# Kernel optimization log

Hardware: AMD Instinct MI355X
Metric: run time of the kernel (lower is better)

The kernel has to match this reference:

```python
import jax, jax.numpy as jnp
import numpy as np

DIM_HEAD = 64
HEADS = 16
EMBED = DIM_HEAD * HEADS
FF = 2 * EMBED
SCALE_BASE = 512.0
LN_EPS = 1e-5
L2_EPS = 1e-12


def setup_inputs() -> dict:
    key = jax.random.key(0)
    ks = jax.random.split(key, 12)
    B, S = 4, 2048
    inp = {
        "Q": jax.random.normal(ks[0], (B, S, EMBED), jnp.float32),
        "K": jax.random.normal(ks[1], (B, S, EMBED), jnp.float32),
        "V": jax.random.normal(ks[2], (B, S, EMBED), jnp.float32),
        "Wqkv": jax.random.normal(ks[3], (EMBED, 3 * EMBED), jnp.float32) * (EMBED ** -0.5),
        "bqkv": jnp.zeros((3 * EMBED,), jnp.float32),
        "q_scale": jnp.ones((DIM_HEAD,), jnp.float32),
        "k_scale": jnp.ones((DIM_HEAD,), jnp.float32),
        "ln_g": jnp.ones((EMBED,), jnp.float32),
        "ln_b": jnp.zeros((EMBED,), jnp.float32),
        "W1": jax.random.normal(ks[4], (EMBED, FF), jnp.float32) * (EMBED ** -0.5),
        "b1": jnp.zeros((FF,), jnp.float32),
        "W2": jax.random.normal(ks[5], (FF, EMBED), jnp.float32) * (FF ** -0.5),
        "b2": jnp.zeros((EMBED,), jnp.float32),
    }
    return inp


def rotate_half(x):
    x1, x2 = jnp.split(x, 2, axis=-1)
    return jnp.concatenate((-x2, x1), axis=-1)


def rotary_tables(seq_len, dim):
    t = jnp.arange(seq_len, dtype=jnp.float32)
    inv_freq = 1.0 / (10000.0 ** (jnp.arange(0, dim, 2, dtype=jnp.float32) / dim))
    freqs = t[:, None] * inv_freq[None, :]            # [S, dim/2]
    freqs = jnp.concatenate((freqs, freqs), axis=-1)  # [S, dim]
    base = (jnp.arange(0, dim, 2, dtype=jnp.float32) + 0.4 * dim) / (1.4 * dim)
    power = (t - seq_len // 2) / SCALE_BASE
    scale = base[None, :] ** power[:, None]           # [S, dim/2]
    scale = jnp.concatenate((scale, scale), axis=-1)  # [S, dim]
    return freqs, scale


def reference(Q, K, V, Wqkv, bqkv, q_scale, k_scale, ln_g, ln_b, W1, b1, W2, b2):
    B, S, D = Q.shape
    dh = q_scale.shape[0]
    H = D // dh

    qkv = Q @ Wqkv + bqkv                              # [B,S,3D]
    qkv = qkv.reshape(B, S, H, 3 * dh).transpose(0, 2, 1, 3)  # [B,H,S,3dh]
    q, k, v = jnp.split(qkv, 3, axis=-1)

    # l2 normalize along head dim (F.normalize semantics)
    q = q / jnp.maximum(jnp.linalg.norm(q, axis=-1, keepdims=True), L2_EPS)
    k = k / jnp.maximum(jnp.linalg.norm(k, axis=-1, keepdims=True), L2_EPS)
    q = q * q_scale
    k = k * k_scale

    freqs, scale = rotary_tables(S, dh)
    cos, sin = jnp.cos(freqs), jnp.sin(freqs)
    q = q * cos * scale + rotate_half(q) * sin * scale
    inv_scale = 1.0 / scale
    k = k * cos * inv_scale + rotate_half(k) * sin * inv_scale

    # scaled dot product attention (non-causal, default scale 1/sqrt(dh))
    logits = jnp.einsum('bhqd,bhkd->bhqk', q, k) / jnp.sqrt(jnp.float32(dh))
    attn = jax.nn.softmax(logits, axis=-1)
    out = jnp.einsum('bhqk,bhkd->bhqd', attn, v)       # [B,H,S,dh]
    out = out.transpose(0, 2, 1, 3).reshape(B, S, D)

    mu = jnp.mean(out, axis=-1, keepdims=True)
    var = jnp.var(out, axis=-1, keepdims=True)
    x = (out - mu) * jax.lax.rsqrt(var + LN_EPS) * ln_g + ln_b

    ff = jax.nn.silu(x @ W1 + b1) @ W2 + b2
    return x + ff
```

## Files before the change

kernel.cpp:

```cpp
#include <hip/hip_runtime.h>
#include <hip/hip_bf16.h>
#include <math.h>


typedef __bf16 bf16_t;
typedef __bf16 bf16x8 __attribute__((ext_vector_type(8)));
typedef _Float16 f16_t;
typedef _Float16 f16x8 __attribute__((ext_vector_type(8)));
typedef float  f32x4  __attribute__((ext_vector_type(4)));

#define B_  4
#define S_  2048
#define H_  16
#define DH_ 64
#define D_  1024
#define FF_ 2048
#define M_  (B_ * S_)

__device__ __forceinline__ float ldx(const void* p, int i, int f) {
    return f ? ((const float*)p)[i] : (float)((const bf16_t*)p)[i];
}
__device__ __forceinline__ float b2f(unsigned short u) {
    return (float)__builtin_bit_cast(bf16_t, u);
}
__device__ __forceinline__ void gll16(const void* g, const void* lds) {
    __builtin_amdgcn_global_load_lds(
        (const __attribute__((address_space(1))) unsigned int*)g,
        (__attribute__((address_space(3))) unsigned int*)lds, 16, 0, 0);
}

__global__ void detect_k(const unsigned short* q, int n, int* flag) {
    const int tid = threadIdx.x;
    float cnt = 0.f;
    for (int i = tid; i < n; i += 256) {
        const int e = (q[i] >> 7) & 0xFF;
        if (e >= 134) cnt += 1.f;
    }
    __shared__ float red[256];
    red[tid] = cnt;
    __syncthreads();
    for (int s = 128; s > 0; s >>= 1) {
        if (tid < s) red[tid] += red[tid + s];
        __syncthreads();
    }
    if (tid == 0) { flag[0] = (red[0] > 0.5f) ? 1 : 0; flag[1] = 1; }
}

__global__ void rope_tables_k(float* __restrict__ ct, float* __restrict__ st,
                              float* __restrict__ sct) {
    const int s = blockIdx.x, i = threadIdx.x;
    const float inv_freq = powf(10000.f, -(float)i / 32.f);
    const float f = (float)s * inv_freq;
    ct[s * 32 + i] = cosf(f);
    st[s * 32 + i] = sinf(f);
    const float base = (2.f * (float)i + 25.6f) / 89.6f;
    const float pw = ((float)s - 1024.f) / 512.f;
    sct[s * 32 + i] = powf(base, pw);
}

__global__ __launch_bounds__(256)
void cvt16_k(const void* __restrict__ in, const int* __restrict__ flag,
             f16_t* __restrict__ o, int n8) {
    const int id = blockIdx.x * 256 + threadIdx.x;
    if (id >= n8) return;
    f16x8 v;
    if (flag[0]) {
        const float4 a = ((const float4*)in)[id * 2];
        const float4 b = ((const float4*)in)[id * 2 + 1];
        v[0] = (f16_t)a.x; v[1] = (f16_t)a.y; v[2] = (f16_t)a.z; v[3] = (f16_t)a.w;
        v[4] = (f16_t)b.x; v[5] = (f16_t)b.y; v[6] = (f16_t)b.z; v[7] = (f16_t)b.w;
    } else {
        const ushort4 a = ((const ushort4*)in)[id * 2];
        const ushort4 b = ((const ushort4*)in)[id * 2 + 1];
        v[0] = (f16_t)b2f(a.x); v[1] = (f16_t)b2f(a.y); v[2] = (f16_t)b2f(a.z); v[3] = (f16_t)b2f(a.w);
        v[4] = (f16_t)b2f(b.x); v[5] = (f16_t)b2f(b.y); v[6] = (f16_t)b2f(b.z); v[7] = (f16_t)b2f(b.w);
    }
    ((f16x8*)o)[id] = v;
}

__global__ __launch_bounds__(256)
void prep_wt16_k(const void* __restrict__ W, const int* __restrict__ flag,
                 f16_t* __restrict__ T16, int K, int N) {
    __shared__ float T[32][33];
    const int tid = threadIdx.x;
    const int n0 = blockIdx.x * 32, k0 = blockIdx.y * 32;
    const int f = flag[0];
#pragma unroll
    for (int i = 0; i < 4; ++i) {
        const int p = i * 256 + tid;
        const int r = p >> 5, c = p & 31;
        T[c][r] = ldx(W, (k0 + r) * N + n0 + c, f);
    }
    __syncthreads();
#pragma unroll
    for (int i = 0; i < 4; ++i) {
        const int p = i * 256 + tid;
        const int r = p >> 5, c = p & 31;
        T16[(size_t)(n0 + r) * K + k0 + c] = (f16_t)T[r][c];
    }
}

template <int ACT, int OUT16, bool RES>
__global__ __launch_bounds__(256)
void gemm16_k(const f16_t* __restrict__ A16, const f16_t* __restrict__ B16,
              const void* __restrict__ bias, const int* __restrict__ fbias,
              const float* __restrict__ resid, float* __restrict__ C,
              f16_t* __restrict__ C16, int M, int N, int K) {
    __shared__ __align__(16) f16_t As[128 * 32];
    __shared__ __align__(16) f16_t Bs[128 * 32];
    const int tid = threadIdx.x;
    const int lane = tid & 63, w = tid >> 6;
    const int l15 = lane & 15, l4 = lane >> 4;
    const int wm = w >> 1, wn = w & 1;
    const int bm = blockIdx.y * 128, bn = blockIdx.x * 128;
    const int sr = lane >> 2, sc = lane & 3;
    const int ck = sc ^ ((sr >> 1) & 3);
    const int rsel = (l15 >> 1) & 3;
    (void)M;

    f32x4 acc[4][4];
#pragma unroll
    for (int i = 0; i < 4; ++i)
#pragma unroll
        for (int j = 0; j < 4; ++j) acc[i][j] = (f32x4){0.f, 0.f, 0.f, 0.f};

    for (int k0 = 0; k0 < K; k0 += 32) {
        __syncthreads();
#pragma unroll
        for (int i = 0; i < 2; ++i) {
            const int t = w * 2 + i;
            const int r = t * 16 + sr;
            gll16(A16 + (size_t)(bm + r) * K + k0 + ck * 8, As + t * 512);
            gll16(B16 + (size_t)(bn + r) * K + k0 + ck * 8, Bs + t * 512);
        }
        __syncthreads();
        f16x8 af[4], bfr[4];
#pragma unroll
        for (int i = 0; i < 4; ++i) {
            const int r = wm * 64 + i * 16 + l15;
            af[i] = *(const f16x8*)&As[r * 32 + ((l4 ^ rsel) << 3)];
        }
#pragma unroll
        for (int j = 0; j < 4; ++j) {
            const int r = wn * 64 + j * 16 + l15;
            bfr[j] = *(const f16x8*)&Bs[r * 32 + ((l4 ^ rsel) << 3)];
        }
#pragma unroll
        for (int i = 0; i < 4; ++i)
#pragma unroll
            for (int j = 0; j < 4; ++j)
                acc[i][j] = __builtin_amdgcn_mfma_f32_16x16x32_f16(af[i], bfr[j], acc[i][j], 0, 0, 0);
    }

    const int fc = fbias[0];
#pragma unroll
    for (int j = 0; j < 4; ++j) {
        const int col = bn + wn * 64 + j * 16 + l15;
        const float bv = ldx(bias, col, fc);
#pragma unroll
        for (int i = 0; i < 4; ++i) {
            const int row0 = bm + wm * 64 + i * 16 + l4 * 4;
#pragma unroll
            for (int r = 0; r < 4; ++r) {
                float t = acc[i][j][r] + bv;
                if constexpr (ACT == 1) t = t / (1.f + expf(-t));
                if constexpr (RES) t += resid[(size_t)(row0 + r) * N + col];
                if constexpr (OUT16) C16[(size_t)(row0 + r) * N + col] = (f16_t)t;
                else                 C[(size_t)(row0 + r) * N + col] = t;
            }
        }
    }
}

__global__ __launch_bounds__(256)
void qkv_post_k(float* __restrict__ qkv,
                const void* __restrict__ qsc, const void* __restrict__ ksc,
                const int* __restrict__ flag,
                const float* __restrict__ ct, const float* __restrict__ st,
                const float* __restrict__ sct, bf16_t* __restrict__ Kb) {
    const int id = blockIdx.x * 256 + threadIdx.x;
    if (id >= M_ * H_) return;
    const int f = flag[0];
    const int bs = id >> 4, h = id & 15;
    const int s = bs & (S_ - 1), b = bs >> 11;
    float* row = qkv + (size_t)bs * (3 * D_) + h * 192;

    float q[DH_];
    float n2 = 0.f;
#pragma unroll
    for (int d = 0; d < DH_; ++d) { q[d] = row[d]; n2 += q[d] * q[d]; }
    float inv = 1.f / fmaxf(sqrtf(n2), 1e-12f);
#pragma unroll
    for (int d = 0; d < DH_; ++d) q[d] *= inv * ldx(qsc, d, f);
#pragma unroll
    for (int d = 0; d < 32; ++d) {
        const float c = ct[s * 32 + d], sn = st[s * 32 + d], sc = sct[s * 32 + d];
        const float a = q[d], bb = q[d + 32];
        q[d]      = (a * c - bb * sn) * sc;
        q[d + 32] = (bb * c + a * sn) * sc;
    }
#pragma unroll
    for (int d = 0; d < DH_; ++d) row[d] = q[d];
    n2 = 0.f;
#pragma unroll
    for (int d = 0; d < DH_; ++d) { q[d] = row[64 + d]; n2 += q[d] * q[d]; }
    inv = 1.f / fmaxf(sqrtf(n2), 1e-12f);
#pragma unroll
    for (int d = 0; d < DH_; ++d) q[d] *= inv * ldx(ksc, d, f);
#pragma unroll
    for (int d = 0; d < 32; ++d) {
        const float c = ct[s * 32 + d], sn = st[s * 32 + d], isc = 1.f / sct[s * 32 + d];
        const float a = q[d], bb = q[d + 32];
        q[d]      = (a * c - bb * sn) * isc;
        q[d + 32] = (bb * c + a * sn) * isc;
    }
    bf16_t* kr = Kb + ((size_t)(b * H_ + h) * S_ + s) * DH_;
#pragma unroll
    for (int d8 = 0; d8 < 8; ++d8) {
        bf16x8 v;
#pragma unroll
        for (int j = 0; j < 8; ++j) v[j] = (bf16_t)q[d8 * 8 + j];
        *(bf16x8*)(kr + d8 * 8) = v;
    }
}

__global__ __launch_bounds__(256)
void vtrans_k(const float* __restrict__ qkv, bf16_t* __restrict__ Vt) {
    __shared__ float T[32][65];
    const int tid = threadIdx.x;
    const int s0 = blockIdx.x * 32;
    const int h  = blockIdx.y;
    const int b  = blockIdx.z;
    {
        const int r = tid >> 3, d0 = (tid & 7) * 8;
        const float* vrow = qkv + (size_t)(b * S_ + s0 + r) * (3 * D_) + h * 192 + 128;
        const float4 a = *(const float4*)(vrow + d0);
        const float4 c = *(const float4*)(vrow + d0 + 4);
        T[r][d0 + 0] = a.x; T[r][d0 + 1] = a.y; T[r][d0 + 2] = a.z; T[r][d0 + 3] = a.w;
        T[r][d0 + 4] = c.x; T[r][d0 + 5] = c.y; T[r][d0 + 6] = c.z; T[r][d0 + 7] = c.w;
    }
    __syncthreads();
    {
        const int d = tid >> 2, sl0 = (tid & 3) * 8;
        bf16x8 o;
#pragma unroll
        for (int j = 0; j < 8; ++j) o[j] = (bf16_t)T[sl0 + j][d];
        *(bf16x8*)(Vt + ((size_t)(b * H_ + h) * DH_ + d) * S_ + s0 + sl0) = o;
    }
}

__global__ __launch_bounds__(256)
void attn_mfma_k(const float* __restrict__ qkv, const bf16_t* __restrict__ Kb,
                 const bf16_t* __restrict__ Vt, float* __restrict__ att) {
    constexpr int RS = 72;
    __shared__ __align__(16) bf16_t Ks[64 * RS];
    __shared__ __align__(16) bf16_t Vs[64 * RS];
    __shared__ __align__(16) bf16_t Ps[4][16 * RS];
    const int tid = threadIdx.x;
    const int lane = tid & 63, w = tid >> 6;
    const int l15 = lane & 15, l4 = lane >> 4;
    const int bid = blockIdx.x;
    const int bh = (bid & 7) * 8 + (bid >> 8);
    const int qt = (bid >> 3) & 31;
    const int b = bh >> 4, h = bh & 15;
    const int q0 = qt * 64 + w * 16;

    bf16x8 qf[2];
    {
        const float* qrow = qkv + (size_t)(b * S_ + q0 + l15) * (3 * D_) + h * 192;
#pragma unroll
        for (int t = 0; t < 2; ++t) {
            const float4 v0 = *(const float4*)(qrow + t * 32 + l4 * 8);
            const float4 v1 = *(const float4*)(qrow + t * 32 + l4 * 8 + 4);
            bf16x8 q8;
            q8[0] = (bf16_t)(v0.x * 0.125f); q8[1] = (bf16_t)(v0.y * 0.125f);
            q8[2] = (bf16_t)(v0.z * 0.125f); q8[3] = (bf16_t)(v0.w * 0.125f);
            q8[4] = (bf16_t)(v1.x * 0.125f); q8[5] = (bf16_t)(v1.y * 0.125f);
            q8[6] = (bf16_t)(v1.z * 0.125f); q8[7] = (bf16_t)(v1.w * 0.125f);
            qf[t] = q8;
        }
    }
    f32x4 of[4];
#pragma unroll
    for (int i = 0; i < 4; ++i) of[i] = (f32x4){0.f, 0.f, 0.f, 0.f};
    float psum[4] = {0.f, 0.f, 0.f, 0.f};

    const bf16_t* Kg = Kb + (size_t)bh * S_ * DH_;
    const bf16_t* Vg = Vt + (size_t)bh * DH_ * S_;
    const int sr = tid >> 2, sc = (tid & 3) * 16;

    for (int j0 = 0; j0 < S_; j0 += 64) {
        __syncthreads();
        *(bf16x8*)&Ks[sr * RS + sc]     = *(const bf16x8*)(Kg + (size_t)(j0 + sr) * DH_ + sc);
        *(bf16x8*)&Ks[sr * RS + sc + 8] = *(const bf16x8*)(Kg + (size_t)(j0 + sr) * DH_ + sc + 8);
        *(bf16x8*)&Vs[sr * RS + sc]     = *(const bf16x8*)(Vg + (size_t)sr * S_ + j0 + sc);
        *(bf16x8*)&Vs[sr * RS + sc + 8] = *(const bf16x8*)(Vg + (size_t)sr * S_ + j0 + sc + 8);
        __syncthreads();

        f32x4 sf[4];
#pragma unroll
        for (int i = 0; i < 4; ++i) sf[i] = (f32x4){0.f, 0.f, 0.f, 0.f};
#pragma unroll
        for (int t = 0; t < 2; ++t)
#pragma unroll
            for (int fj = 0; fj < 4; ++fj) {
                const bf16x8 kf = *(const bf16x8*)&Ks[(fj * 16 + l15) * RS + t * 32 + l4 * 8];
                sf[fj] = __builtin_amdgcn_mfma_f32_16x16x32_bf16(qf[t], kf, sf[fj], 0, 0, 0);
            }
#pragma unroll
        for (int fj = 0; fj < 4; ++fj)
#pragma unroll
            for (int r = 0; r < 4; ++r) {
                const float p = __expf(sf[fj][r]);
                const bf16_t pb = (bf16_t)p;
                psum[r] += (float)pb;
                Ps[w][(l4 * 4 + r) * RS + fj * 16 + l15] = pb;
            }
#pragma unroll
        for (int t = 0; t < 2; ++t) {
            const bf16x8 pf = *(const bf16x8*)&Ps[w][l15 * RS + t * 32 + l4 * 8];
#pragma unroll
            for (int fd = 0; fd < 4; ++fd) {
                const bf16x8 vf = *(const bf16x8*)&Vs[(fd * 16 + l15) * RS + t * 32 + l4 * 8];
                of[fd] = __builtin_amdgcn_mfma_f32_16x16x32_bf16(pf, vf, of[fd], 0, 0, 0);
            }
        }
    }
#pragma unroll
    for (int r = 0; r < 4; ++r)
#pragma unroll
        for (int msk = 1; msk < 16; msk <<= 1) psum[r] += __shfl_xor(psum[r], msk);
#pragma unroll
    for (int r = 0; r < 4; ++r) {
        const float inv = 1.f / psum[r];
        float* orow = att + (size_t)(b * S_ + q0 + l4 * 4 + r) * D_ + h * DH_;
#pragma unroll
        for (int fd = 0; fd < 4; ++fd) orow[fd * 16 + l15] = of[fd][r] * inv;
    }
}

__global__ __launch_bounds__(256)
void layernorm_k(const float* __restrict__ in, const void* __restrict__ g,
                 const void* __restrict__ be, const int* __restrict__ flag,
                 float* __restrict__ xo, f16_t* __restrict__ x16) {
    const int row = blockIdx.x, tid = threadIdx.x;
    const int lane = tid & 63, wave = tid >> 6;
    const int f = flag[0];
    const float* r = in + (size_t)row * D_;
    float v[4], s = 0.f, ss = 0.f;
#pragma unroll
    for (int i = 0; i < 4; ++i) {
        v[i] = r[tid + i * 256];
        s += v[i]; ss += v[i] * v[i];
    }
#pragma unroll
    for (int msk = 1; msk < 64; msk <<= 1) { s += __shfl_xor(s, msk); ss += __shfl_xor(ss, msk); }
    __shared__ float rs[4], rss[4];
    if (lane == 0) { rs[wave] = s; rss[wave] = ss; }
    __syncthreads();
    s = rs[0] + rs[1] + rs[2] + rs[3];
    ss = rss[0] + rss[1] + rss[2] + rss[3];
    const float mu = s * (1.f / (float)D_);
    const float var = fmaxf(ss * (1.f / (float)D_) - mu * mu, 0.f);
    const float inv = rsqrtf(var + 1e-5f);
    float* xr = xo + (size_t)row * D_;
    f16_t* hr = x16 + (size_t)row * D_;
#pragma unroll
    for (int i = 0; i < 4; ++i) {
        const int c = tid + i * 256;
        const float t = (v[i] - mu) * inv * ldx(g, c, f) + ldx(be, c, f);
        xr[c] = t;
        hr[c] = (f16_t)t;
    }
}

__global__ void host_marker_k(int code, float* __restrict__ out) {
    if (code != 0) out[0] = 1e10f * (float)(1 + code);
}

extern "C" void kernel_launch(void* const* d_in, const int* in_sizes, int n_in,
                              void* d_out, int out_size, void* d_ws, size_t ws_size,
                              hipStream_t stream) {
    (void)out_size;
    const void* Q    = d_in[0];
    const void* Wqkv = d_in[3];
    const void* bqkv = d_in[4];
    const void* qsc  = d_in[5];
    const void* ksc  = d_in[6];
    const void* ln_g = d_in[7];
    const void* ln_b = d_in[8];
    const void* W1   = d_in[9];
    const void* b1   = d_in[10];
    const void* W2   = d_in[11];
    const void* b2   = d_in[12];

    constexpr size_t OFF_QKV  = 0;
    constexpr size_t OFF_X    = 0;
    constexpr size_t OFF_X16  = 33554432;
    constexpr size_t OFF_H16  = 50331648;
    constexpr size_t OFF_WQ16 = 100663296;
    constexpr size_t OFF_W116 = 106954752;
    constexpr size_t OFF_W216 = 111149056;
    constexpr size_t OFF_Q16  = 115343360;
    constexpr size_t OFF_KB   = 115343360;
    constexpr size_t OFF_VT   = 132120576;
    constexpr size_t OFF_RC   = 148897792;
    constexpr size_t OFF_RS   = OFF_RC + 262144;
    constexpr size_t OFF_RSC  = OFF_RS + 262144;
    constexpr size_t OFF_FLAG = OFF_RSC + 262144;
    constexpr size_t WS_NEED  = OFF_FLAG + 64;

    float* out = (float*)d_out;
    char* ws = (char*)d_ws;
    float*  qkv   = (float*)(ws + OFF_QKV);
    float*  xbuf  = (float*)(ws + OFF_X);
    f16_t*  x16   = (f16_t*)(ws + OFF_X16);
    f16_t*  h16   = (f16_t*)(ws + OFF_H16);
    f16_t*  wq16  = (f16_t*)(ws + OFF_WQ16);
    f16_t*  w116  = (f16_t*)(ws + OFF_W116);
    f16_t*  w216  = (f16_t*)(ws + OFF_W216);
    f16_t*  q16   = (f16_t*)(ws + OFF_Q16);
    bf16_t* kb    = (bf16_t*)(ws + OFF_KB);
    bf16_t* vtb   = (bf16_t*)(ws + OFF_VT);
    float*  rc    = (float*)(ws + OFF_RC);
    float*  rsn   = (float*)(ws + OFF_RS);
    float*  rsc   = (float*)(ws + OFF_RSC);
    int*    flag  = (int*)(ws + OFF_FLAG);

    int err_stage = 0;
    (void)hipGetLastError();
    #define LCHK(stage) do { if (hipGetLastError() != hipSuccess && err_stage == 0) err_stage = (stage); } while (0)

    if (n_in != 13) err_stage = 90;
    else if (in_sizes[0] != 8388608 || in_sizes[3] != 3145728 || in_sizes[4] != 3072 ||
             in_sizes[5] != 64 || in_sizes[7] != 1024 || in_sizes[9] != 2097152 ||
             in_sizes[10] != 2048 || in_sizes[11] != 2097152 || in_sizes[12] != 1024)
        err_stage = 91;
    else if (ws_size < WS_NEED) err_stage = 92;
    if (err_stage != 0) {
        host_marker_k<<<1, 1, 0, stream>>>(err_stage, out);
        return;
    }

    detect_k<<<1, 256, 0, stream>>>((const unsigned short*)Q, 65536, flag);        LCHK(1);
    rope_tables_k<<<S_, 32, 0, stream>>>(rc, rsn, rsc);                            LCHK(2);
    cvt16_k<<<(M_ * D_ / 8) / 256, 256, 0, stream>>>(Q, flag, q16, M_ * D_ / 8);   LCHK(3);
    prep_wt16_k<<<dim3(3 * D_ / 32, D_ / 32), 256, 0, stream>>>(
        Wqkv, flag, wq16, D_, 3 * D_);                                             LCHK(4);
    prep_wt16_k<<<dim3(FF_ / 32, D_ / 32), 256, 0, stream>>>(
        W1, flag, w116, D_, FF_);                                                  LCHK(5);
    prep_wt16_k<<<dim3(D_ / 32, FF_ / 32), 256, 0, stream>>>(
        W2, flag, w216, FF_, D_);                                                  LCHK(6);
    gemm16_k<0, 0, false><<<dim3(3 * D_ / 128, M_ / 128), 256, 0, stream>>>(
        q16, wq16, bqkv, flag, nullptr, qkv, nullptr, M_, 3 * D_, D_);             LCHK(7);
    qkv_post_k<<<(M_ * H_) / 256, 256, 0, stream>>>(
        qkv, qsc, ksc, flag, rc, rsn, rsc, kb);                                    LCHK(8);
    vtrans_k<<<dim3(S_ / 32, H_, B_), 256, 0, stream>>>(qkv, vtb);                 LCHK(9);
    attn_mfma_k<<<B_ * H_ * (S_ / 64), 256, 0, stream>>>(qkv, kb, vtb, out);       LCHK(10);
    layernorm_k<<<M_, 256, 0, stream>>>(out, ln_g, ln_b, flag, xbuf, x16);         LCHK(11);
    gemm16_k<1, 1, false><<<dim3(FF_ / 128, M_ / 128), 256, 0, stream>>>(
        x16, w116, b1, flag, nullptr, nullptr, h16, M_, FF_, D_);                  LCHK(12);
    gemm16_k<0, 0, true><<<dim3(D_ / 128, M_ / 128), 256, 0, stream>>>(
        h16, w216, b2, flag, xbuf, out, nullptr, M_, D_, FF_);                     LCHK(13);
    host_marker_k<<<1, 1, 0, stream>>>(err_stage, out);
    #undef LCHK
}
```

Before: 658.8 us.

## Store QKV in fp16, pre-scale Q to bf16, double-buffer attention K/V with async loads

The QKV GEMM now writes fp16 instead of fp32, and the post-processing kernel writes Q as pre-scaled bf16 in a head-major layout. The attention kernel therefore reads compact Q directly and stages K/V with direct global-to-LDS loads into a double buffer. The LDS tiles use XOR swizzles instead of padding, and the MFMA sections get wave priority hints. LayerNorm no longer writes an fp32 copy, and the final GEMM takes its residual from the fp16 normalized tensor. Together these cut memory traffic and overlap loads with compute, at the cost of some precision in the QKV intermediate and the residual.

```diff
diff --git a/kernel.cpp b/kernel.cpp
--- a/kernel.cpp
+++ b/kernel.cpp
@@ -100,12 +100,12 @@
     }
 }
 
-template <int ACT, int OUT16, bool RES>
+template <int ACT, int OUT16, int RES>
 __global__ __launch_bounds__(256)
 void gemm16_k(const f16_t* __restrict__ A16, const f16_t* __restrict__ B16,
               const void* __restrict__ bias, const int* __restrict__ fbias,
-              const float* __restrict__ resid, float* __restrict__ C,
-              f16_t* __restrict__ C16, int M, int N, int K) {
+              const float* __restrict__ residf, const f16_t* __restrict__ resid16,
+              float* __restrict__ C, f16_t* __restrict__ C16, int M, int N, int K) {
     __shared__ __align__(16) f16_t As[128 * 32];
     __shared__ __align__(16) f16_t Bs[128 * 32];
     const int tid = threadIdx.x;
@@ -164,7 +164,8 @@
             for (int r = 0; r < 4; ++r) {
                 float t = acc[i][j][r] + bv;
                 if constexpr (ACT == 1) t = t / (1.f + expf(-t));
-                if constexpr (RES) t += resid[(size_t)(row0 + r) * N + col];
+                if constexpr (RES == 1) t += residf[(size_t)(row0 + r) * N + col];
+                if constexpr (RES == 2) t += (float)resid16[(size_t)(row0 + r) * N + col];
                 if constexpr (OUT16) C16[(size_t)(row0 + r) * N + col] = (f16_t)t;
                 else                 C[(size_t)(row0 + r) * N + col] = t;
             }
@@ -173,22 +174,27 @@
 }
 
 __global__ __launch_bounds__(256)
-void qkv_post_k(float* __restrict__ qkv,
+void qkv_post_k(const f16_t* __restrict__ qkv16,
                 const void* __restrict__ qsc, const void* __restrict__ ksc,
                 const int* __restrict__ flag,
                 const float* __restrict__ ct, const float* __restrict__ st,
-                const float* __restrict__ sct, bf16_t* __restrict__ Kb) {
+                const float* __restrict__ sct,
+                bf16_t* __restrict__ Qb, bf16_t* __restrict__ Kb) {
     const int id = blockIdx.x * 256 + threadIdx.x;
     if (id >= M_ * H_) return;
     const int f = flag[0];
     const int bs = id >> 4, h = id & 15;
     const int s = bs & (S_ - 1), b = bs >> 11;
-    float* row = qkv + (size_t)bs * (3 * D_) + h * 192;
+    const f16_t* row = qkv16 + (size_t)bs * (3 * D_) + h * 192;
 
     float q[DH_];
     float n2 = 0.f;
 #pragma unroll
-    for (int d = 0; d < DH_; ++d) { q[d] = row[d]; n2 += q[d] * q[d]; }
+    for (int d8 = 0; d8 < 8; ++d8) {
+        const f16x8 v = *(const f16x8*)(row + d8 * 8);
+#pragma unroll
+        for (int j = 0; j < 8; ++j) { q[d8 * 8 + j] = (float)v[j]; n2 += q[d8*8+j]*q[d8*8+j]; }
+    }
     float inv = 1.f / fmaxf(sqrtf(n2), 1e-12f);
 #pragma unroll
     for (int d = 0; d < DH_; ++d) q[d] *= inv * ldx(qsc, d, f);
@@ -199,11 +205,21 @@
         q[d]      = (a * c - bb * sn) * sc;
         q[d + 32] = (bb * c + a * sn) * sc;
     }
-#pragma unroll
-    for (int d = 0; d < DH_; ++d) row[d] = q[d];
+    bf16_t* qr = Qb + ((size_t)(b * H_ + h) * S_ + s) * DH_;
+#pragma unroll
+    for (int d8 = 0; d8 < 8; ++d8) {
+        bf16x8 v;
+#pragma unroll
+        for (int j = 0; j < 8; ++j) v[j] = (bf16_t)(q[d8 * 8 + j] * 0.125f);
+        *(bf16x8*)(qr + d8 * 8) = v;
+    }
     n2 = 0.f;
 #pragma unroll
-    for (int d = 0; d < DH_; ++d) { q[d] = row[64 + d]; n2 += q[d] * q[d]; }
+    for (int d8 = 0; d8 < 8; ++d8) {
+        const f16x8 v = *(const f16x8*)(row + 64 + d8 * 8);
+#pragma unroll
+        for (int j = 0; j < 8; ++j) { q[d8 * 8 + j] = (float)v[j]; n2 += q[d8*8+j]*q[d8*8+j]; }
+    }
     inv = 1.f / fmaxf(sqrtf(n2), 1e-12f);
 #pragma unroll
     for (int d = 0; d < DH_; ++d) q[d] *= inv * ldx(ksc, d, f);
@@ -225,7 +241,7 @@
 }
 
 __global__ __launch_bounds__(256)
-void vtrans_k(const float* __restrict__ qkv, bf16_t* __restrict__ Vt) {
+void vtrans_k(const f16_t* __restrict__ qkv16, bf16_t* __restrict__ Vt) {
     __shared__ float T[32][65];
     const int tid = threadIdx.x;
     const int s0 = blockIdx.x * 32;
@@ -233,11 +249,10 @@
     const int b  = blockIdx.z;
     {
         const int r = tid >> 3, d0 = (tid & 7) * 8;
-        const float* vrow = qkv + (size_t)(b * S_ + s0 + r) * (3 * D_) + h * 192 + 128;
-        const float4 a = *(const float4*)(vrow + d0);
-        const float4 c = *(const float4*)(vrow + d0 + 4);
-        T[r][d0 + 0] = a.x; T[r][d0 + 1] = a.y; T[r][d0 + 2] = a.z; T[r][d0 + 3] = a.w;
-        T[r][d0 + 4] = c.x; T[r][d0 + 5] = c.y; T[r][d0 + 6] = c.z; T[r][d0 + 7] = c.w;
+        const f16_t* vrow = qkv16 + (size_t)(b * S_ + s0 + r) * (3 * D_) + h * 192 + 128;
+        const f16x8 v = *(const f16x8*)(vrow + d0);
+#pragma unroll
+        for (int j = 0; j < 8; ++j) T[r][d0 + j] = (float)v[j];
     }
     __syncthreads();
     {
@@ -250,12 +265,11 @@
 }
 
 __global__ __launch_bounds__(256)
-void attn_mfma_k(const float* __restrict__ qkv, const bf16_t* __restrict__ Kb,
+void attn_mfma_k(const bf16_t* __restrict__ Qb, const bf16_t* __restrict__ Kb,
                  const bf16_t* __restrict__ Vt, float* __restrict__ att) {
-    constexpr int RS = 72;
-    __shared__ __align__(16) bf16_t Ks[64 * RS];
-    __shared__ __align__(16) bf16_t Vs[64 * RS];
-    __shared__ __align__(16) bf16_t Ps[4][16 * RS];
+    __shared__ __align__(16) bf16_t Ks[2][64 * 64];
+    __shared__ __align__(16) bf16_t Vs[2][64 * 64];
+    __shared__ __align__(16) bf16_t Ps[4][16 * 64];
     const int tid = threadIdx.x;
     const int lane = tid & 63, w = tid >> 6;
     const int l15 = lane & 15, l4 = lane >> 4;
@@ -265,48 +279,51 @@
     const int b = bh >> 4, h = bh & 15;
     const int q0 = qt * 64 + w * 16;
 
+    const bf16_t* Qg = Qb + (size_t)bh * S_ * DH_;
+    const bf16_t* Kg = Kb + (size_t)bh * S_ * DH_;
+    const bf16_t* Vg = Vt + (size_t)bh * DH_ * S_;
+
     bf16x8 qf[2];
-    {
-        const float* qrow = qkv + (size_t)(b * S_ + q0 + l15) * (3 * D_) + h * 192;
-#pragma unroll
-        for (int t = 0; t < 2; ++t) {
-            const float4 v0 = *(const float4*)(qrow + t * 32 + l4 * 8);
-            const float4 v1 = *(const float4*)(qrow + t * 32 + l4 * 8 + 4);
-            bf16x8 q8;
-            q8[0] = (bf16_t)(v0.x * 0.125f); q8[1] = (bf16_t)(v0.y * 0.125f);
-            q8[2] = (bf16_t)(v0.z * 0.125f); q8[3] = (bf16_t)(v0.w * 0.125f);
-            q8[4] = (bf16_t)(v1.x * 0.125f); q8[5] = (bf16_t)(v1.y * 0.125f);
-            q8[6] = (bf16_t)(v1.z * 0.125f); q8[7] = (bf16_t)(v1.w * 0.125f);
-            qf[t] = q8;
-        }
-    }
+#pragma unroll
+    for (int t = 0; t < 2; ++t)
+        qf[t] = *(const bf16x8*)(Qg + (size_t)(q0 + l15) * DH_ + t * 32 + l4 * 8);
+
     f32x4 of[4];
 #pragma unroll
     for (int i = 0; i < 4; ++i) of[i] = (f32x4){0.f, 0.f, 0.f, 0.f};
     float psum[4] = {0.f, 0.f, 0.f, 0.f};
 
-    const bf16_t* Kg = Kb + (size_t)bh * S_ * DH_;
-    const bf16_t* Vg = Vt + (size_t)bh * DH_ * S_;
-    const int sr = tid >> 2, sc = (tid & 3) * 16;
-
-    for (int j0 = 0; j0 < S_; j0 += 64) {
-        __syncthreads();
-        *(bf16x8*)&Ks[sr * RS + sc]     = *(const bf16x8*)(Kg + (size_t)(j0 + sr) * DH_ + sc);
-        *(bf16x8*)&Ks[sr * RS + sc + 8] = *(const bf16x8*)(Kg + (size_t)(j0 + sr) * DH_ + sc + 8);
-        *(bf16x8*)&Vs[sr * RS + sc]     = *(const bf16x8*)(Vg + (size_t)sr * S_ + j0 + sc);
-        *(bf16x8*)&Vs[sr * RS + sc + 8] = *(const bf16x8*)(Vg + (size_t)sr * S_ + j0 + sc + 8);
-        __syncthreads();
-
+    const int srow = lane >> 3;
+    const int sck  = (lane & 7) ^ (srow & 7);
+
+#define STAGE(bufi, j0) do {                                                        \
+    _Pragma("unroll")                                                               \
+    for (int i_ = 0; i_ < 2; ++i_) {                                                \
+        const int rbase = w * 16 + i_ * 8;                                          \
+        const int rr = rbase + srow;                                                \
+        gll16(Kg + (size_t)((j0) + rr) * DH_ + sck * 8, &Ks[bufi][rbase * 64]);     \
+        gll16(Vg + (size_t)rr * S_ + (j0) + sck * 8, &Vs[bufi][rbase * 64]);        \
+    } } while (0)
+
+    STAGE(0, 0);
+    __syncthreads();
+    int cur = 0;
+    for (int jt = 0; jt < S_ / 64; ++jt) {
+        if (jt < S_ / 64 - 1) STAGE(cur ^ 1, (jt + 1) * 64);
         f32x4 sf[4];
 #pragma unroll
         for (int i = 0; i < 4; ++i) sf[i] = (f32x4){0.f, 0.f, 0.f, 0.f};
-#pragma unroll
-        for (int t = 0; t < 2; ++t)
+        __builtin_amdgcn_s_setprio(1);
+#pragma unroll
+        for (int t = 0; t < 2; ++t) {
+            const int rsl = ((t * 4 + l4) ^ (l15 & 7)) << 3;
 #pragma unroll
             for (int fj = 0; fj < 4; ++fj) {
-                const bf16x8 kf = *(const bf16x8*)&Ks[(fj * 16 + l15) * RS + t * 32 + l4 * 8];
+                const bf16x8 kf = *(const bf16x8*)&Ks[cur][(fj * 16 + l15) * 64 + rsl];
                 sf[fj] = __builtin_amdgcn_mfma_f32_16x16x32_bf16(qf[t], kf, sf[fj], 0, 0, 0);
             }
+        }
+        __builtin_amdgcn_s_setprio(0);
 #pragma unroll
         for (int fj = 0; fj < 4; ++fj)
 #pragma unroll
@@ -314,18 +331,27 @@
                 const float p = __expf(sf[fj][r]);
                 const bf16_t pb = (bf16_t)p;
                 psum[r] += (float)pb;
-                Ps[w][(l4 * 4 + r) * RS + fj * 16 + l15] = pb;
+                const int q = l4 * 4 + r;
+                const int slot = (fj * 2 + (l15 >> 3)) ^ ((q >> 1) & 7);
+                Ps[w][q * 64 + slot * 8 + (l15 & 7)] = pb;
             }
+        __builtin_amdgcn_s_setprio(1);
 #pragma unroll
         for (int t = 0; t < 2; ++t) {
-            const bf16x8 pf = *(const bf16x8*)&Ps[w][l15 * RS + t * 32 + l4 * 8];
+            const int pslot = ((t * 4 + l4) ^ ((l15 >> 1) & 7)) << 3;
+            const bf16x8 pf = *(const bf16x8*)&Ps[w][l15 * 64 + pslot];
+            const int rsl = ((t * 4 + l4) ^ (l15 & 7)) << 3;
 #pragma unroll
             for (int fd = 0; fd < 4; ++fd) {
-                const bf16x8 vf = *(const bf16x8*)&Vs[(fd * 16 + l15) * RS + t * 32 + l4 * 8];
+                const bf16x8 vf = *(const bf16x8*)&Vs[cur][(fd * 16 + l15) * 64 + rsl];
                 of[fd] = __builtin_amdgcn_mfma_f32_16x16x32_bf16(pf, vf, of[fd], 0, 0, 0);
             }
         }
-    }
+        __builtin_amdgcn_s_setprio(0);
+        __syncthreads();
+        cur ^= 1;
+    }
+#undef STAGE
 #pragma unroll
     for (int r = 0; r < 4; ++r)
 #pragma unroll
@@ -342,7 +368,7 @@
 __global__ __launch_bounds__(256)
 void layernorm_k(const float* __restrict__ in, const void* __restrict__ g,
                  const void* __restrict__ be, const int* __restrict__ flag,
-                 float* __restrict__ xo, f16_t* __restrict__ x16) {
+                 f16_t* __restrict__ x16) {
     const int row = blockIdx.x, tid = threadIdx.x;
     const int lane = tid & 63, wave = tid >> 6;
     const int f = flag[0];
@@ -363,14 +389,11 @@
     const float mu = s * (1.f / (float)D_);
     const float var = fmaxf(ss * (1.f / (float)D_) - mu * mu, 0.f);
     const float inv = rsqrtf(var + 1e-5f);
-    float* xr = xo + (size_t)row * D_;
     f16_t* hr = x16 + (size_t)row * D_;
 #pragma unroll
     for (int i = 0; i < 4; ++i) {
         const int c = tid + i * 256;
-        const float t = (v[i] - mu) * inv * ldx(g, c, f) + ldx(be, c, f);
-        xr[c] = t;
-        hr[c] = (f16_t)t;
+        hr[c] = (f16_t)((v[i] - mu) * inv * ldx(g, c, f) + ldx(be, c, f));
     }
 }
 
@@ -394,34 +417,36 @@
     const void* W2   = d_in[11];
     const void* b2   = d_in[12];
 
-    constexpr size_t OFF_QKV  = 0;
-    constexpr size_t OFF_X    = 0;
-    constexpr size_t OFF_X16  = 33554432;
-    constexpr size_t OFF_H16  = 50331648;
-    constexpr size_t OFF_WQ16 = 100663296;
-    constexpr size_t OFF_W116 = 106954752;
-    constexpr size_t OFF_W216 = 111149056;
-    constexpr size_t OFF_Q16  = 115343360;
-    constexpr size_t OFF_KB   = 115343360;
-    constexpr size_t OFF_VT   = 132120576;
-    constexpr size_t OFF_RC   = 148897792;
-    constexpr size_t OFF_RS   = OFF_RC + 262144;
-    constexpr size_t OFF_RSC  = OFF_RS + 262144;
-    constexpr size_t OFF_FLAG = OFF_RSC + 262144;
-    constexpr size_t WS_NEED  = OFF_FLAG + 64;
+    constexpr size_t OFF_QKV16 = 0;
+    constexpr size_t OFF_ATT   = 0;
+    constexpr size_t OFF_X16   = 33554432;
+    constexpr size_t OFF_H16   = 50331648;
+    constexpr size_t OFF_Q16   = 83886080;
+    constexpr size_t OFF_QB    = 83886080;
+    constexpr size_t OFF_KB    = 100663296;
+    constexpr size_t OFF_VT    = 117440512;
+    constexpr size_t OFF_WQ16  = 134217728;
+    constexpr size_t OFF_W116  = 140509184;
+    constexpr size_t OFF_W216  = 144703488;
+    constexpr size_t OFF_RC    = 148897792;
+    constexpr size_t OFF_RS    = OFF_RC + 262144;
+    constexpr size_t OFF_RSC   = OFF_RS + 262144;
+    constexpr size_t OFF_FLAG  = OFF_RSC + 262144;
+    constexpr size_t WS_NEED   = OFF_FLAG + 64;
 
     float* out = (float*)d_out;
     char* ws = (char*)d_ws;
-    float*  qkv   = (float*)(ws + OFF_QKV);
-    float*  xbuf  = (float*)(ws + OFF_X);
+    f16_t*  qkv16 = (f16_t*)(ws + OFF_QKV16);
+    float*  attb  = (float*)(ws + OFF_ATT);
     f16_t*  x16   = (f16_t*)(ws + OFF_X16);
     f16_t*  h16   = (f16_t*)(ws + OFF_H16);
+    f16_t*  q16   = (f16_t*)(ws + OFF_Q16);
+    bf16_t* qb    = (bf16_t*)(ws + OFF_QB);
+    bf16_t* kb    = (bf16_t*)(ws + OFF_KB);
+    bf16_t* vtb   = (bf16_t*)(ws + OFF_VT);
     f16_t*  wq16  = (f16_t*)(ws + OFF_WQ16);
     f16_t*  w116  = (f16_t*)(ws + OFF_W116);
     f16_t*  w216  = (f16_t*)(ws + OFF_W216);
-    f16_t*  q16   = (f16_t*)(ws + OFF_Q16);
-    bf16_t* kb    = (bf16_t*)(ws + OFF_KB);
-    bf16_t* vtb   = (bf16_t*)(ws + OFF_VT);
     float*  rc    = (float*)(ws + OFF_RC);
     float*  rsn   = (float*)(ws + OFF_RS);
     float*  rsc   = (float*)(ws + OFF_RSC);
@@ -451,17 +476,17 @@
         W1, flag, w116, D_, FF_);                                                  LCHK(5);
     prep_wt16_k<<<dim3(D_ / 32, FF_ / 32), 256, 0, stream>>>(
         W2, flag, w216, FF_, D_);                                                  LCHK(6);
-    gemm16_k<0, 0, false><<<dim3(3 * D_ / 128, M_ / 128), 256, 0, stream>>>(
-        q16, wq16, bqkv, flag, nullptr, qkv, nullptr, M_, 3 * D_, D_);             LCHK(7);
+    gemm16_k<0, 1, 0><<<dim3(3 * D_ / 128, M_ / 128), 256, 0, stream>>>(
+        q16, wq16, bqkv, flag, nullptr, nullptr, nullptr, qkv16, M_, 3 * D_, D_);  LCHK(7);
     qkv_post_k<<<(M_ * H_) / 256, 256, 0, stream>>>(
-        qkv, qsc, ksc, flag, rc, rsn, rsc, kb);                                    LCHK(8);
-    vtrans_k<<<dim3(S_ / 32, H_, B_), 256, 0, stream>>>(qkv, vtb);                 LCHK(9);
-    attn_mfma_k<<<B_ * H_ * (S_ / 64), 256, 0, stream>>>(qkv, kb, vtb, out);       LCHK(10);
-    layernorm_k<<<M_, 256, 0, stream>>>(out, ln_g, ln_b, flag, xbuf, x16);         LCHK(11);
-    gemm16_k<1, 1, false><<<dim3(FF_ / 128, M_ / 128), 256, 0, stream>>>(
-        x16, w116, b1, flag, nullptr, nullptr, h16, M_, FF_, D_);                  LCHK(12);
-    gemm16_k<0, 0, true><<<dim3(D_ / 128, M_ / 128), 256, 0, stream>>>(
-        h16, w216, b2, flag, xbuf, out, nullptr, M_, D_, FF_);                     LCHK(13);
+        qkv16, qsc, ksc, flag, rc, rsn, rsc, qb, kb);                              LCHK(8);
+    vtrans_k<<<dim3(S_ / 32, H_, B_), 256, 0, stream>>>(qkv16, vtb);               LCHK(9);
+    attn_mfma_k<<<B_ * H_ * (S_ / 64), 256, 0, stream>>>(qb, kb, vtb, attb);       LCHK(10);
+    layernorm_k<<<M_, 256, 0, stream>>>(attb, ln_g, ln_b, flag, x16);              LCHK(11);
+    gemm16_k<1, 1, 0><<<dim3(FF_ / 128, M_ / 128), 256, 0, stream>>>(
+        x16, w116, b1, flag, nullptr, nullptr, nullptr, h16, M_, FF_, D_);         LCHK(12);
+    gemm16_k<0, 0, 2><<<dim3(D_ / 128, M_ / 128), 256, 0, stream>>>(
+        h16, w216, b2, flag, nullptr, x16, out, nullptr, M_, D_, FF_);             LCHK(13);
     host_marker_k<<<1, 1, 0, stream>>>(err_stage, out);
     #undef LCHK
 }
```

Result: faster. 637.8 us (-3.2%).
